# Optimization experiments

Measured on AMD Instinct MI355X. Metric: run time of the kernel, lower is better.

The kernel has to match this reference:

```python
import jax, jax.numpy as jnp
import numpy as np

NUM_EMBEDDINGS = 8192
EMBEDDING_DIM = 512
COMMITMENT_COST = 0.25
N_INPUTS = 32768


def setup_inputs() -> dict:
    key = jax.random.key(0)
    k1, k2 = jax.random.split(key)
    inputs = jax.random.normal(k1, (N_INPUTS, EMBEDDING_DIM), dtype=jnp.float32)
    weight = jax.random.normal(k2, (NUM_EMBEDDINGS, EMBEDDING_DIM), dtype=jnp.float32)
    return {"inputs": inputs, "weight": weight}


def reference(inputs, weight):
    # distances[n, k] = ||x_n||^2 + ||w_k||^2 - 2 x_n . w_k   -> [N, K]
    distances = (
        jnp.sum(inputs ** 2, axis=1, keepdims=True)
        + jnp.sum(weight ** 2, axis=1)
        - 2.0 * (inputs @ weight.T)
    )
    probs = jax.nn.softmax(-distances, axis=-1)            # [N, K]
    idx = jnp.argmin(distances, axis=1)                    # [N]
    quantized = weight[idx]                                # gather == one-hot @ weight

    e_latent_loss = jnp.mean((jax.lax.stop_gradient(quantized) - inputs) ** 2)
    q_latent_loss = jnp.mean((quantized - jax.lax.stop_gradient(inputs)) ** 2)
    loss = q_latent_loss + COMMITMENT_COST * e_latent_loss

    # straight-through estimator
    quantized_st = inputs + jax.lax.stop_gradient(quantized - inputs)

    # avg over one-hot encodings == normalized code histogram
    counts = jnp.bincount(idx, length=NUM_EMBEDDINGS).astype(inputs.dtype)
    avg_probs = counts / inputs.shape[0]
    perplexity = jnp.exp(-jnp.sum(avg_probs * jnp.log(avg_probs + 1e-10)))

    return (quantized_st, probs, loss, perplexity)
```

## Files before the change

### kernel.cpp

```cpp
#include <hip/hip_runtime.h>
#include <hip/hip_fp16.h>
#include <math.h>

#define N_ROWS 32768
#define K_CODES 8192
#define DIM 512

#define OUT_Q 0
#define OUT_P ((size_t)N_ROWS * DIM)
#define OUT_LOSS (OUT_P + (size_t)N_ROWS * K_CODES)
#define OUT_PERP (OUT_LOSS + 1)

#define WS_WSQ 0
#define WS_CNT (K_CODES)
#define WS_ERR (2 * K_CODES)
#define WS_F16 (2 * K_CODES + N_ROWS)

#define XH_OFF ((size_t)0)
#define XL_OFF ((size_t)N_ROWS * DIM)
#define WH_OFF ((size_t)2 * N_ROWS * DIM)
#define WL_OFF ((size_t)2 * N_ROWS * DIM + (size_t)K_CODES * DIM)
#define F16_COUNT ((size_t)2 * (N_ROWS + K_CODES) * DIM)
#define WS_NEEDED ((size_t)WS_F16 * 4 + F16_COUNT * 2)

typedef _Float16 f16x8 __attribute__((ext_vector_type(8)));
typedef float f32x4 __attribute__((ext_vector_type(4)));

__device__ inline void load_lds16(const void* g, void* l) {
    __builtin_amdgcn_global_load_lds((const __attribute__((address_space(1))) void*)g,
                                     (__attribute__((address_space(3))) void*)l,
                                     16, 0, 0);
}

__device__ inline unsigned int fkey(float f) {
    unsigned int b = __float_as_uint(f);
    return b ^ ((unsigned int)((int)b >> 31) | 0x80000000u);
}
__device__ inline float fkey_inv(unsigned int k) {
    unsigned int b = (k & 0x80000000u) ? (k ^ 0x80000000u) : ~k;
    return __uint_as_float(b);
}

__global__ void wsq_kernel(const float* __restrict__ W, float* __restrict__ ws) {
    int row = blockIdx.x;
    int lane = threadIdx.x;
    const float* src = W + (size_t)row * DIM;
    float4 v0 = *(const float4*)(src + lane * 8);
    float4 v1 = *(const float4*)(src + lane * 8 + 4);
    float s = v0.x * v0.x + v0.y * v0.y + v0.z * v0.z + v0.w * v0.w
            + v1.x * v1.x + v1.y * v1.y + v1.z * v1.z + v1.w * v1.w;
#pragma unroll
    for (int off = 32; off > 0; off >>= 1) s += __shfl_down(s, off, 64);
    if (lane == 0) ws[WS_WSQ + row] = s;
}

__global__ void __launch_bounds__(256) convert_split_kernel(
    const float* __restrict__ X, const float* __restrict__ W,
    _Float16* __restrict__ f16base, float* __restrict__ ws) {
    const size_t NX8 = (size_t)N_ROWS * DIM / 8;
    size_t t = (size_t)blockIdx.x * 256 + threadIdx.x;
    const float* src;
    _Float16 *hd, *ld;
    bool isW = (t >= NX8);
    if (!isW) {
        src = X + t * 8;
        hd = f16base + XH_OFF + t * 8;
        ld = f16base + XL_OFF + t * 8;
    } else {
        size_t u = t - NX8;
        src = W + u * 8;
        hd = f16base + WH_OFF + u * 8;
        ld = f16base + WL_OFF + u * 8;
    }
    float4 v0 = *(const float4*)src;
    float4 v1 = *(const float4*)(src + 4);
    float v[8] = {v0.x, v0.y, v0.z, v0.w, v1.x, v1.y, v1.z, v1.w};
    f16x8 h, l;
    float s = 0.f;
#pragma unroll
    for (int i = 0; i < 8; ++i) {
        _Float16 hv = (_Float16)v[i];
        h[i] = hv;
        l[i] = (_Float16)(v[i] - (float)hv);
        s += v[i] * v[i];
    }
    *(f16x8*)hd = h;
    *(f16x8*)ld = l;
    if (isW) {
#pragma unroll
        for (int off = 32; off > 0; off >>= 1) s += __shfl_down(s, off, 64);
        if ((threadIdx.x & 63) == 0) ws[WS_WSQ + ((t - NX8) >> 6)] = s;
    }
}

#define LDSB 24576
#define AH_O 0
#define AL_O 8192
#define BH_O 16384
#define BL_O 20480

__global__ void __launch_bounds__(512, 2) gemm_dist_mfma_kernel(
    const _Float16* __restrict__ f16base, const float* __restrict__ ws,
    float* __restrict__ out) {
    __shared__ _Float16 lds[3 * LDSB];

    const int tid = threadIdx.x;
    const int w = tid >> 6;
    const int lane = tid & 63;

    int lin = blockIdx.y * 64 + blockIdx.x;
    int swz = (lin & 7) * 1024 + (lin >> 3);
    const int bn = (swz & 63) * 128;
    const int bm = (swz >> 6) * 256;

    const int wr = w >> 1;
    const int wc = w & 1;
    const int q = lane >> 4;
    const int fm = lane & 15;
    const int l4 = lane >> 2;
    const int p = lane & 3;

    f32x4 acc[4][4];
#pragma unroll
    for (int i = 0; i < 4; ++i)
#pragma unroll
        for (int j = 0; j < 4; ++j) acc[i][j] = (f32x4){0.f, 0.f, 0.f, 0.f};

    auto stage = [&](int ks, _Float16* buf, int part) {
        const int kk = ks * 32;
        int g = w * 2 + part;
        int arow = g * 16 + l4;
        int ca = p ^ ((arow >> 1) & 3);
        size_t aoff = (size_t)(bm + arow) * DIM + kk + ca * 8;
        load_lds16(f16base + XH_OFF + aoff, buf + AH_O + g * 512);
        load_lds16(f16base + XL_OFF + aoff, buf + AL_O + g * 512);
        int brow = w * 16 + l4;
        int cb = p ^ ((brow >> 1) & 3);
        size_t boff = (size_t)(bn + brow) * DIM + kk + cb * 8;
        if (part == 0)
            load_lds16(f16base + WH_OFF + boff, buf + BH_O + w * 512);
        else
            load_lds16(f16base + WL_OFF + boff, buf + BL_O + w * 512);
    };

    _Float16* c0 = lds;
    _Float16* c1 = lds + LDSB;
    _Float16* c2 = lds + 2 * LDSB;

    stage(0, c0, 0); stage(0, c0, 1);
    stage(1, c1, 0); stage(1, c1, 1);
    asm volatile("s_waitcnt vmcnt(6)" ::: "memory");
    __builtin_amdgcn_s_barrier();
    __builtin_amdgcn_sched_barrier(0);

#pragma unroll 1
    for (int ks = 0; ks < 16; ++ks) {
        f16x8 bhv[4], blv[4];
#pragma unroll
        for (int j = 0; j < 4; ++j) {
            int bb = wc * 64 + j * 16 + fm;
            int off = bb * 32 + ((q ^ ((bb >> 1) & 3)) * 8);
            bhv[j] = *(const f16x8*)&c0[BH_O + off];
            blv[j] = *(const f16x8*)&c0[BL_O + off];
        }
        f16x8 ah[2], al[2];
#pragma unroll
        for (int i = 0; i < 2; ++i) {
            int am = wr * 64 + i * 16 + fm;
            int off = am * 32 + ((q ^ ((am >> 1) & 3)) * 8);
            ah[i] = *(const f16x8*)&c0[AH_O + off];
            al[i] = *(const f16x8*)&c0[AL_O + off];
        }
        if (ks < 14) stage(ks + 2, c2, 0);
        __builtin_amdgcn_s_setprio(1);
#pragma unroll
        for (int i = 0; i < 2; ++i)
#pragma unroll
            for (int j = 0; j < 4; ++j) {
                acc[i][j] = __builtin_amdgcn_mfma_f32_16x16x32_f16(
                    ah[i], bhv[j], acc[i][j], 0, 0, 0);
                acc[i][j] = __builtin_amdgcn_mfma_f32_16x16x32_f16(
                    ah[i], blv[j], acc[i][j], 0, 0, 0);
                acc[i][j] = __builtin_amdgcn_mfma_f32_16x16x32_f16(
                    al[i], bhv[j], acc[i][j], 0, 0, 0);
            }
        __builtin_amdgcn_s_setprio(0);
        __builtin_amdgcn_s_barrier();
        __builtin_amdgcn_sched_barrier(0);

#pragma unroll
        for (int i = 0; i < 2; ++i) {
            int am = wr * 64 + (i + 2) * 16 + fm;
            int off = am * 32 + ((q ^ ((am >> 1) & 3)) * 8);
            ah[i] = *(const f16x8*)&c0[AH_O + off];
            al[i] = *(const f16x8*)&c0[AL_O + off];
        }
        if (ks < 14) stage(ks + 2, c2, 1);
        __builtin_amdgcn_s_setprio(1);
#pragma unroll
        for (int i = 0; i < 2; ++i)
#pragma unroll
            for (int j = 0; j < 4; ++j) {
                acc[i + 2][j] = __builtin_amdgcn_mfma_f32_16x16x32_f16(
                    ah[i], bhv[j], acc[i + 2][j], 0, 0, 0);
                acc[i + 2][j] = __builtin_amdgcn_mfma_f32_16x16x32_f16(
                    ah[i], blv[j], acc[i + 2][j], 0, 0, 0);
                acc[i + 2][j] = __builtin_amdgcn_mfma_f32_16x16x32_f16(
                    al[i], bhv[j], acc[i + 2][j], 0, 0, 0);
            }
        __builtin_amdgcn_s_setprio(0);
        if (ks < 14) {
            asm volatile("s_waitcnt vmcnt(6)" ::: "memory");
        } else if (ks == 14) {
            asm volatile("s_waitcnt vmcnt(0)" ::: "memory");
        }
        __builtin_amdgcn_s_barrier();
        __builtin_amdgcn_sched_barrier(0);

        _Float16* t0 = c0; c0 = c1; c1 = c2; c2 = t0;
    }

    const float* wsq = ws + WS_WSQ;
    float* Dout = out + OUT_P;
    const int q4 = q * 4;
#pragma unroll
    for (int i = 0; i < 4; ++i) {
#pragma unroll
        for (int j = 0; j < 4; ++j) {
            int n = bn + wc * 64 + j * 16 + fm;
            float wn = wsq[n];
#pragma unroll
            for (int r = 0; r < 4; ++r) {
                int m = bm + wr * 64 + i * 16 + q4 + r;
                Dout[(size_t)m * K_CODES + n] = wn - 2.f * acc[i][j][r];
            }
        }
    }
}

#define BM 128
#define BN 128
#define BK 16

__global__ void __launch_bounds__(256) gemm_dist_fp32_kernel(
    const float* __restrict__ X, const float* __restrict__ W,
    const float* __restrict__ ws, float* __restrict__ out) {
    __shared__ float As[BK][BM];
    __shared__ float Bs[BK][BN];

    const int bn = blockIdx.x * BN;
    const int bm = blockIdx.y * BM;
    const int tid = threadIdx.x;
    const int tx = tid & 15;
    const int ty = tid >> 4;
    const int lr = tid >> 1;
    const int lc = (tid & 1) * 8;

    float acc[8][8];
#pragma unroll
    for (int i = 0; i < 8; ++i)
#pragma unroll
        for (int j = 0; j < 8; ++j) acc[i][j] = 0.f;

    const float* aptr = X + (size_t)(bm + lr) * DIM + lc;
    const float* bptr = W + (size_t)(bn + lr) * DIM + lc;

    for (int k0 = 0; k0 < DIM; k0 += BK) {
        float4 a0 = *(const float4*)(aptr + k0);
        float4 a1 = *(const float4*)(aptr + k0 + 4);
        float4 b0 = *(const float4*)(bptr + k0);
        float4 b1 = *(const float4*)(bptr + k0 + 4);
        __syncthreads();
        As[lc + 0][lr] = a0.x; As[lc + 1][lr] = a0.y;
        As[lc + 2][lr] = a0.z; As[lc + 3][lr] = a0.w;
        As[lc + 4][lr] = a1.x; As[lc + 5][lr] = a1.y;
        As[lc + 6][lr] = a1.z; As[lc + 7][lr] = a1.w;
        Bs[lc + 0][lr] = b0.x; Bs[lc + 1][lr] = b0.y;
        Bs[lc + 2][lr] = b0.z; Bs[lc + 3][lr] = b0.w;
        Bs[lc + 4][lr] = b1.x; Bs[lc + 5][lr] = b1.y;
        Bs[lc + 6][lr] = b1.z; Bs[lc + 7][lr] = b1.w;
        __syncthreads();
#pragma unroll
        for (int kk = 0; kk < BK; ++kk) {
            float a[8], b[8];
            *(float4*)&a[0] = *(const float4*)&As[kk][ty * 8];
            *(float4*)&a[4] = *(const float4*)&As[kk][ty * 8 + 4];
            *(float4*)&b[0] = *(const float4*)&Bs[kk][tx * 8];
            *(float4*)&b[4] = *(const float4*)&Bs[kk][tx * 8 + 4];
#pragma unroll
            for (int i = 0; i < 8; ++i)
#pragma unroll
                for (int j = 0; j < 8; ++j)
                    acc[i][j] = fmaf(a[i], b[j], acc[i][j]);
        }
    }

    const float* wsq = ws + WS_WSQ;
    const int m0 = bm + ty * 8;
    const int n0 = bn + tx * 8;
    float wn[8];
    *(float4*)&wn[0] = *(const float4*)(wsq + n0);
    *(float4*)&wn[4] = *(const float4*)(wsq + n0 + 4);
    float* Dout = out + OUT_P;
#pragma unroll
    for (int i = 0; i < 8; ++i) {
        float4 o0, o1;
        o0.x = wn[0] - 2.f * acc[i][0];
        o0.y = wn[1] - 2.f * acc[i][1];
        o0.z = wn[2] - 2.f * acc[i][2];
        o0.w = wn[3] - 2.f * acc[i][3];
        o1.x = wn[4] - 2.f * acc[i][4];
        o1.y = wn[5] - 2.f * acc[i][5];
        o1.z = wn[6] - 2.f * acc[i][6];
        o1.w = wn[7] - 2.f * acc[i][7];
        float* drow = Dout + (size_t)(m0 + i) * K_CODES + n0;
        *(float4*)(drow) = o0;
        *(float4*)(drow + 4) = o1;
    }
}

__global__ void __launch_bounds__(256) probs_quant_kernel(
    const float* __restrict__ X, const float* __restrict__ W,
    float* __restrict__ out, float* __restrict__ ws) {
    const int n = blockIdx.x;
    const int tid = threadIdx.x;
    __shared__ unsigned long long mred[4];
    __shared__ float fred[4];

    float4* Drow4 = (float4*)(out + OUT_P + (size_t)n * K_CODES);

    float4 e[8];
    unsigned long long best = ~0ull;
#pragma unroll
    for (int t = 0; t < 8; ++t) {
        float4 v = Drow4[tid + t * 256];
        e[t] = v;
        unsigned int c0 = (unsigned int)((tid + t * 256) * 4);
        unsigned long long k;
        k = ((unsigned long long)fkey(v.x) << 32) | (c0 + 0u);
        best = k < best ? k : best;
        k = ((unsigned long long)fkey(v.y) << 32) | (c0 + 1u);
        best = k < best ? k : best;
        k = ((unsigned long long)fkey(v.z) << 32) | (c0 + 2u);
        best = k < best ? k : best;
        k = ((unsigned long long)fkey(v.w) << 32) | (c0 + 3u);
        best = k < best ? k : best;
    }
#pragma unroll
    for (int d = 1; d < 64; d <<= 1) {
        unsigned long long o = __shfl_xor(best, d, 64);
        best = o < best ? o : best;
    }
    if ((tid & 63) == 0) mred[tid >> 6] = best;
    __syncthreads();
    unsigned long long bm = mred[0];
    bm = mred[1] < bm ? mred[1] : bm;
    bm = mred[2] < bm ? mred[2] : bm;
    bm = mred[3] < bm ? mred[3] : bm;
    const float smin = fkey_inv((unsigned int)(bm >> 32));
    const int amin = (int)(bm & 0xFFFFFFFFu);

    float sum = 0.f;
#pragma unroll
    for (int t = 0; t < 8; ++t) {
        float4 v = e[t];
        float4 ev;
        ev.x = __expf(smin - v.x);
        ev.y = __expf(smin - v.y);
        ev.z = __expf(smin - v.z);
        ev.w = __expf(smin - v.w);
        e[t] = ev;
        sum += ev.x + ev.y + ev.z + ev.w;
    }
#pragma unroll
    for (int off = 32; off > 0; off >>= 1) sum += __shfl_down(sum, off, 64);
    if ((tid & 63) == 0) fred[tid >> 6] = sum;
    __syncthreads();
    const float inv = 1.0f / (fred[0] + fred[1] + fred[2] + fred[3]);

#pragma unroll
    for (int t = 0; t < 8; ++t) {
        float4 ev = e[t];
        ev.x *= inv; ev.y *= inv; ev.z *= inv; ev.w *= inv;
        Drow4[tid + t * 256] = ev;
    }

    const float2* xr = (const float2*)(X + (size_t)n * DIM);
    const float2* wr = (const float2*)(W + (size_t)amin * DIM);
    float2* qr = (float2*)(out + OUT_Q + (size_t)n * DIM);
    float2 x = xr[tid];
    float2 qv = wr[tid];
    float2 d2, o;
    d2.x = qv.x - x.x; d2.y = qv.y - x.y;
    o.x = x.x + d2.x;  o.y = x.y + d2.y;
    qr[tid] = o;
    float err = d2.x * d2.x + d2.y * d2.y;
#pragma unroll
    for (int off = 32; off > 0; off >>= 1) err += __shfl_down(err, off, 64);
    __syncthreads();
    if ((tid & 63) == 0) fred[tid >> 6] = err;
    __syncthreads();
    if (tid == 0) {
        ws[WS_ERR + n] = fred[0] + fred[1] + fred[2] + fred[3];
        atomicAdd(ws + WS_CNT + amin, 1.0f);
    }
}

__global__ void __launch_bounds__(1024) finalize_kernel(
    float* __restrict__ out, const float* __restrict__ ws) {
    __shared__ float red[1024];
    const int tid = threadIdx.x;

    float errsum = 0.f;
    for (int j = tid; j < N_ROWS; j += 1024) errsum += ws[WS_ERR + j];
    red[tid] = errsum;
    __syncthreads();
    for (int st = 512; st > 0; st >>= 1) {
        if (tid < st) red[tid] += red[tid + st];
        __syncthreads();
    }
    const float total_err = red[0];
    __syncthreads();

    float ent = 0.f;
    for (int j = tid; j < K_CODES; j += 1024) {
        float p = ws[WS_CNT + j] * (1.0f / (float)N_ROWS);
        ent -= p * logf(p + 1e-10f);
    }
    red[tid] = ent;
    __syncthreads();
    for (int st = 512; st > 0; st >>= 1) {
        if (tid < st) red[tid] += red[tid + st];
        __syncthreads();
    }
    if (tid == 0) {
        float mse = total_err * (1.0f / ((float)N_ROWS * (float)DIM));
        out[OUT_LOSS] = mse + 0.25f * mse;
        out[OUT_PERP] = expf(red[0]);
    }
}

extern "C" void kernel_launch(void* const* d_in, const int* in_sizes, int n_in,
                              void* d_out, int out_size, void* d_ws, size_t ws_size,
                              hipStream_t stream) {
    const float* X = (const float*)d_in[0];
    const float* W = (const float*)d_in[1];
    float* out = (float*)d_out;
    float* ws = (float*)d_ws;

    hipMemsetAsync(ws + WS_CNT, 0, K_CODES * sizeof(float), stream);

    if (ws_size >= WS_NEEDED) {
        _Float16* f16base = (_Float16*)(ws + WS_F16);
        const int conv_blocks =
            (int)(((size_t)(N_ROWS + K_CODES) * DIM / 8 + 255) / 256);
        convert_split_kernel<<<conv_blocks, 256, 0, stream>>>(X, W, f16base, ws);

        dim3 ggrid(64, 128);
        gemm_dist_mfma_kernel<<<ggrid, 512, 0, stream>>>(f16base, ws, out);
    } else {
        wsq_kernel<<<K_CODES, 64, 0, stream>>>(W, ws);
        dim3 ggrid(K_CODES / BN, N_ROWS / BM);
        gemm_dist_fp32_kernel<<<ggrid, 256, 0, stream>>>(X, W, ws, out);
    }

    probs_quant_kernel<<<N_ROWS, 256, 0, stream>>>(X, W, out, ws);
    finalize_kernel<<<1, 1024, 0, stream>>>(out, ws);
}
```

Measured before the change: 2.311 ms.

## Split MFMA loop into four A-fragment clusters with barriers and remap XCD tiles

The GEMM main loop now reads one A fragment pair at a time and runs its 12 MFMAs as a cluster. Each cluster is bracketed by barriers and an lgkmcnt wait, which interleaves LDS reads with matrix work across waves in a ping-pong style and lowers register pressure from holding two A fragments. The block-to-tile mapping is changed so each XCD handles a contiguous group of 8 column tiles, meant to improve L2 reuse of W. The probs kernel also issues the X row load early to hide its latency. The extra barriers add synchronisation cost, which could outweigh the gains.

```diff
diff --git a/kernel.cpp b/kernel.cpp
--- a/kernel.cpp
+++ b/kernel.cpp
@@ -109,9 +109,10 @@
     const int lane = tid & 63;
 
     int lin = blockIdx.y * 64 + blockIdx.x;
-    int swz = (lin & 7) * 1024 + (lin >> 3);
-    const int bn = (swz & 63) * 128;
-    const int bm = (swz >> 6) * 256;
+    int xcd = lin & 7;
+    int idx = lin >> 3;
+    const int bn = (xcd * 8 + (idx & 7)) * 128;
+    const int bm = (idx >> 3) * 256;
 
     const int wr = w >> 1;
     const int wc = w & 1;
@@ -156,6 +157,25 @@
 #pragma unroll 1
     for (int ks = 0; ks < 16; ++ks) {
         f16x8 bhv[4], blv[4];
+
+        auto readA = [&](int i, f16x8& h, f16x8& l) {
+            int am = wr * 64 + i * 16 + fm;
+            int off = am * 32 + ((q ^ ((am >> 1) & 3)) * 8);
+            h = *(const f16x8*)&c0[AH_O + off];
+            l = *(const f16x8*)&c0[AL_O + off];
+        };
+        auto cluster = [&](int i, f16x8 h, f16x8 l) {
+#pragma unroll
+            for (int j = 0; j < 4; ++j) {
+                acc[i][j] = __builtin_amdgcn_mfma_f32_16x16x32_f16(
+                    h, bhv[j], acc[i][j], 0, 0, 0);
+                acc[i][j] = __builtin_amdgcn_mfma_f32_16x16x32_f16(
+                    h, blv[j], acc[i][j], 0, 0, 0);
+                acc[i][j] = __builtin_amdgcn_mfma_f32_16x16x32_f16(
+                    l, bhv[j], acc[i][j], 0, 0, 0);
+            }
+        };
+
 #pragma unroll
         for (int j = 0; j < 4; ++j) {
             int bb = wc * 64 + j * 16 + fm;
@@ -163,51 +183,45 @@
             bhv[j] = *(const f16x8*)&c0[BH_O + off];
             blv[j] = *(const f16x8*)&c0[BL_O + off];
         }
-        f16x8 ah[2], al[2];
-#pragma unroll
-        for (int i = 0; i < 2; ++i) {
-            int am = wr * 64 + i * 16 + fm;
-            int off = am * 32 + ((q ^ ((am >> 1) & 3)) * 8);
-            ah[i] = *(const f16x8*)&c0[AH_O + off];
-            al[i] = *(const f16x8*)&c0[AL_O + off];
-        }
+        f16x8 a0h, a0l;
+        readA(0, a0h, a0l);
         if (ks < 14) stage(ks + 2, c2, 0);
+        __builtin_amdgcn_s_barrier();
+        asm volatile("s_waitcnt lgkmcnt(0)" ::: "memory");
+        __builtin_amdgcn_sched_barrier(0);
         __builtin_amdgcn_s_setprio(1);
-#pragma unroll
-        for (int i = 0; i < 2; ++i)
-#pragma unroll
-            for (int j = 0; j < 4; ++j) {
-                acc[i][j] = __builtin_amdgcn_mfma_f32_16x16x32_f16(
-                    ah[i], bhv[j], acc[i][j], 0, 0, 0);
-                acc[i][j] = __builtin_amdgcn_mfma_f32_16x16x32_f16(
-                    ah[i], blv[j], acc[i][j], 0, 0, 0);
-                acc[i][j] = __builtin_amdgcn_mfma_f32_16x16x32_f16(
-                    al[i], bhv[j], acc[i][j], 0, 0, 0);
-            }
+        cluster(0, a0h, a0l);
         __builtin_amdgcn_s_setprio(0);
         __builtin_amdgcn_s_barrier();
+
+        f16x8 a1h, a1l;
+        readA(1, a1h, a1l);
+        __builtin_amdgcn_s_barrier();
+        asm volatile("s_waitcnt lgkmcnt(0)" ::: "memory");
         __builtin_amdgcn_sched_barrier(0);
-
-#pragma unroll
-        for (int i = 0; i < 2; ++i) {
-            int am = wr * 64 + (i + 2) * 16 + fm;
-            int off = am * 32 + ((q ^ ((am >> 1) & 3)) * 8);
-            ah[i] = *(const f16x8*)&c0[AH_O + off];
-            al[i] = *(const f16x8*)&c0[AL_O + off];
-        }
+        __builtin_amdgcn_s_setprio(1);
+        cluster(1, a1h, a1l);
+        __builtin_amdgcn_s_setprio(0);
+        __builtin_amdgcn_s_barrier();
+
+        f16x8 a2h, a2l;
+        readA(2, a2h, a2l);
         if (ks < 14) stage(ks + 2, c2, 1);
+        __builtin_amdgcn_s_barrier();
+        asm volatile("s_waitcnt lgkmcnt(0)" ::: "memory");
+        __builtin_amdgcn_sched_barrier(0);
         __builtin_amdgcn_s_setprio(1);
-#pragma unroll
-        for (int i = 0; i < 2; ++i)
-#pragma unroll
-            for (int j = 0; j < 4; ++j) {
-                acc[i + 2][j] = __builtin_amdgcn_mfma_f32_16x16x32_f16(
-                    ah[i], bhv[j], acc[i + 2][j], 0, 0, 0);
-                acc[i + 2][j] = __builtin_amdgcn_mfma_f32_16x16x32_f16(
-                    ah[i], blv[j], acc[i + 2][j], 0, 0, 0);
-                acc[i + 2][j] = __builtin_amdgcn_mfma_f32_16x16x32_f16(
-                    al[i], bhv[j], acc[i + 2][j], 0, 0, 0);
-            }
+        cluster(2, a2h, a2l);
+        __builtin_amdgcn_s_setprio(0);
+        __builtin_amdgcn_s_barrier();
+
+        f16x8 a3h, a3l;
+        readA(3, a3h, a3l);
+        __builtin_amdgcn_s_barrier();
+        asm volatile("s_waitcnt lgkmcnt(0)" ::: "memory");
+        __builtin_amdgcn_sched_barrier(0);
+        __builtin_amdgcn_s_setprio(1);
+        cluster(3, a3h, a3l);
         __builtin_amdgcn_s_setprio(0);
         if (ks < 14) {
             asm volatile("s_waitcnt vmcnt(6)" ::: "memory");
@@ -329,6 +343,9 @@
 
     float4* Drow4 = (float4*)(out + OUT_P + (size_t)n * K_CODES);
 
+    const float2* xr = (const float2*)(X + (size_t)n * DIM);
+    float2 x = xr[tid];
+
     float4 e[8];
     unsigned long long best = ~0ull;
 #pragma unroll
@@ -385,10 +402,8 @@
         Drow4[tid + t * 256] = ev;
     }
 
-    const float2* xr = (const float2*)(X + (size_t)n * DIM);
     const float2* wr = (const float2*)(W + (size_t)amin * DIM);
     float2* qr = (float2*)(out + OUT_Q + (size_t)n * DIM);
-    float2 x = xr[tid];
     float2 qv = wr[tid];
     float2 d2, o;
     d2.x = qv.x - x.x; d2.y = qv.y - x.y;
```

Result: no change. 2.350 ms (+1.7%).
